# Performance work log

Hardware: AMD Instinct MI355X
Metric: run time of the kernel (lower is better)

The kernel has to match this reference:

```python
import jax, jax.numpy as jnp
import numpy as np

N, E, L, D, ED, M = 100000, 1600000, 4, 64, 16, 128
BN_EPS = 1e-5


def _bn(x, w, b):
    # BatchNorm1d in training mode: biased batch stats over the node dim
    m = x.mean(0)
    v = jnp.mean((x - m) ** 2, axis=0)
    return (x - m) * jax.lax.rsqrt(v + BN_EPS) * w + b


def _leaky(x):
    return jnp.where(x > 0, x, 0.01 * x)  # torch LeakyReLU default slope


def setup_inputs() -> dict:
    key = jax.random.key(0)
    ks = jax.random.split(key, 8)
    s = 0.05
    return {
        "x": jax.random.normal(ks[0], (N, D), jnp.float32),
        "edge_index": jax.random.randint(ks[1], (2, E), 0, N, jnp.int32),
        "edge_attr": jax.random.normal(ks[2], (E, ED), jnp.float32),
        "bn_pre_w": jnp.ones((L, D), jnp.float32),
        "bn_pre_b": jnp.zeros((L, D), jnp.float32),
        "edge_lin_w": jax.random.normal(ks[3], (L, D, ED), jnp.float32) * s,
        "edge_lin_b": jnp.zeros((L, D), jnp.float32),
        "lin1_w": jax.random.normal(ks[4], (L, D, D), jnp.float32) * s,
        "lin1_b": jnp.zeros((L, D), jnp.float32),
        "bn_mid_w": jnp.ones((L, D), jnp.float32),
        "bn_mid_b": jnp.zeros((L, D), jnp.float32),
        "lin2_w": jax.random.normal(ks[5], (L, D, D), jnp.float32) * s,
        "lin2_b": jnp.zeros((L, D), jnp.float32),
        "eps": jnp.zeros((L,), jnp.float32),
        "cls1_w": jax.random.normal(ks[6], (M, D), jnp.float32) * s,
        "cls1_b": jnp.zeros((M,), jnp.float32),
        "cls_bn_w": jnp.ones((M,), jnp.float32),
        "cls_bn_b": jnp.zeros((M,), jnp.float32),
        "cls2_w": jax.random.normal(ks[7], (1, M), jnp.float32) * s,
        "cls2_b": jnp.zeros((1,), jnp.float32),
    }


def reference(x, edge_index, edge_attr, bn_pre_w, bn_pre_b, edge_lin_w, edge_lin_b,
              lin1_w, lin1_b, bn_mid_w, bn_mid_b, lin2_w, lin2_b, eps,
              cls1_w, cls1_b, cls_bn_w, cls_bn_b, cls2_w, cls2_b):
    src, dst = edge_index[0], edge_index[1]
    h = x
    for i in range(L):  # fixed, small layer count
        hn = _bn(h, bn_pre_w[i], bn_pre_b[i])
        hi = hn if i == 0 else _leaky(hn)
        # GINEConv: msg = relu(x_src + Lin(edge_attr)); sum-aggregate at dst
        e = edge_attr @ edge_lin_w[i].T + edge_lin_b[i]            # [E, D]
        msg = jax.nn.relu(hi[src] + e)                              # gather [E, D]
        aggr = jax.ops.segment_sum(msg, dst, num_segments=N)        # scatter [N, D]
        z = (1.0 + eps[i]) * hi + aggr
        # nn: Linear -> BN -> LeakyReLU -> Linear
        z = z @ lin1_w[i].T + lin1_b[i]
        z = _leaky(_bn(z, bn_mid_w[i], bn_mid_b[i]))
        z = z @ lin2_w[i].T + lin2_b[i]
        h = z if i == 0 else h + z  # residual (skipped on first layer)
    y = _leaky(_bn(h @ cls1_w.T + cls1_b, cls_bn_w, cls_bn_b))
    y = y @ cls2_w.T + cls2_b
    return y.reshape(-1)  # torch.flatten -> [N]
```

## Files before the change

kernel.cpp:

```cpp
#include <hip/hip_runtime.h>
#include <hip/hip_bf16.h>

constexpr int GN = 100000;
constexpr int GE = 1600000;
constexpr float FN = 100000.0f;
constexpr float BN_EPS = 1e-5f;

typedef __attribute__((ext_vector_type(8))) short bf16x8;
typedef __attribute__((ext_vector_type(4))) float f32x4;
typedef __bf16 bfp2 __attribute__((ext_vector_type(2)));

#if __has_builtin(__builtin_amdgcn_fdot2_f32_bf16)
#define HAVE_DOT2 1
#else
#define HAVE_DOT2 0
#endif

__device__ __forceinline__ unsigned packbf2(float a, float b) {
    __hip_bfloat162 h = __float22bfloat162_rn(float2{a, b});
    union { __hip_bfloat162 h2; unsigned u; } cv;
    cv.h2 = h;
    return cv.u;
}

__device__ __forceinline__ unsigned short bf16rn(float f) {
    unsigned u = __builtin_bit_cast(unsigned, f);
    unsigned r = (u + 0x7FFF + ((u >> 16) & 1)) >> 16;
    return (unsigned short)r;
}

__device__ __forceinline__ float bflo(unsigned u) {
    return __builtin_bit_cast(float, u << 16);
}
__device__ __forceinline__ float bfhi(unsigned u) {
    return __builtin_bit_cast(float, u & 0xFFFF0000u);
}
__device__ __forceinline__ float bfu16(unsigned short u) {
    return __builtin_bit_cast(float, (unsigned)u << 16);
}


__global__ __launch_bounds__(256) void hist_kernel(const int* __restrict__ dst,
                                                   int* __restrict__ deg) {
    for (int i = blockIdx.x * blockDim.x + threadIdx.x; i < GE; i += gridDim.x * blockDim.x)
        atomicAdd(&deg[dst[i]], 1);
}

__global__ __launch_bounds__(256) void bsum_kernel(const int* __restrict__ deg,
                                                   int* __restrict__ bsum,
                                                   const float* __restrict__ l1w,
                                                   const float* __restrict__ l2w,
                                                   const float* __restrict__ c1w,
                                                   unsigned short* __restrict__ wb) {
    int b = blockIdx.x;
    int i0 = b * 1024 + threadIdx.x * 4;
    int s = 0;
#pragma unroll
    for (int k = 0; k < 4; ++k) {
        int i = i0 + k;
        if (i < GN) s += deg[i];
    }
    for (int o = 32; o >= 1; o >>= 1) s += __shfl_down(s, o, 64);
    __shared__ int ws[4];
    if ((threadIdx.x & 63) == 0) ws[threadIdx.x >> 6] = s;
    __syncthreads();
    if (threadIdx.x == 0) bsum[b] = ws[0] + ws[1] + ws[2] + ws[3];
    for (int i = b * 256 + threadIdx.x; i < 40960; i += gridDim.x * 256) {
        float v;
        if (i < 16384) v = l1w[i];
        else if (i < 32768) v = l2w[i - 16384];
        else v = c1w[i - 32768];
        wb[i] = bf16rn(v);
    }
}

__global__ void bscan_kernel(const int* __restrict__ bsum, int* __restrict__ bbase,
                             int* __restrict__ offEnd, int nb) {
    int t = threadIdx.x;
    int carry = 0;
    for (int base = 0; base < nb; base += 64) {
        int v = (base + t < nb) ? bsum[base + t] : 0;
        int incl = v;
        for (int o = 1; o < 64; o <<= 1) {
            int u = __shfl_up(incl, o, 64);
            if (t >= o) incl += u;
        }
        if (base + t < nb) bbase[base + t] = carry + incl - v;
        carry += __shfl(incl, 63, 64);
    }
    if (t == 0) offEnd[0] = carry;
}

__global__ __launch_bounds__(256) void bscatter_kernel(int* __restrict__ deg,
                                                       const int* __restrict__ bbase,
                                                       int* __restrict__ off) {
    int b = blockIdx.x;
    int t = threadIdx.x;
    int i0 = b * 1024 + t * 4;
    int v[4];
    int s = 0;
#pragma unroll
    for (int k = 0; k < 4; ++k) {
        int i = i0 + k;
        v[k] = (i < GN) ? deg[i] : 0;
        s += v[k];
    }
    int incl = s;
    int lane = t & 63;
    for (int o = 1; o < 64; o <<= 1) {
        int u = __shfl_up(incl, o, 64);
        if (lane >= o) incl += u;
    }
    __shared__ int wsum[4];
    if (lane == 63) wsum[t >> 6] = incl;
    __syncthreads();
    int w = t >> 6;
    int wb = 0;
#pragma unroll
    for (int k = 0; k < 4; ++k)
        if (k < w) wb += wsum[k];
    int ex = bbase[b] + wb + incl - s;
#pragma unroll
    for (int k = 0; k < 4; ++k) {
        int i = i0 + k;
        if (i < GN) { off[i] = ex; deg[i] = ex; }
        ex += v[k];
    }
}

__global__ __launch_bounds__(256) void fill_sorted_kernel(
    const int* __restrict__ src, const int* __restrict__ dst,
    const float4* __restrict__ attr,
    int* __restrict__ cursor,
    int* __restrict__ srcS, unsigned* __restrict__ attrS,
    float* __restrict__ zeroBuf) {
    if (blockIdx.x == 0 && threadIdx.x < 128) zeroBuf[threadIdx.x] = 0.f;
    for (int i = blockIdx.x * blockDim.x + threadIdx.x; i < GE; i += gridDim.x * blockDim.x) {
        int pos = atomicAdd(&cursor[dst[i]], 1);
        srcS[pos] = src[i];
        size_t r = (size_t)i * 4;
        float4 a0 = attr[r], a1 = attr[r + 1], a2 = attr[r + 2], a3 = attr[r + 3];
        uint4 ua, ub;
        ua.x = packbf2(a0.x, a0.y); ua.y = packbf2(a0.z, a0.w);
        ua.z = packbf2(a1.x, a1.y); ua.w = packbf2(a1.z, a1.w);
        ub.x = packbf2(a2.x, a2.y); ub.y = packbf2(a2.z, a2.w);
        ub.z = packbf2(a3.x, a3.y); ub.w = packbf2(a3.z, a3.w);
        uint4* out = (uint4*)(attrS + (size_t)pos * 8);
        out[0] = ua;
        out[1] = ub;
    }
}


__global__ __launch_bounds__(256) void col_stats64(const float* __restrict__ in,
                                                   float* __restrict__ sum,
                                                   float* __restrict__ sq,
                                                   unsigned short* __restrict__ outb) {
    int c = threadIdx.x & 63;
    int lr = threadIdx.x >> 6;
    float s = 0.f, q = 0.f;
    for (int r = blockIdx.x * 4 + lr; r < GN; r += gridDim.x * 4) {
        float v = in[(size_t)r * 64 + c];
        s += v;
        q += v * v;
        outb[(size_t)r * 64 + c] = bf16rn(v);
    }
    __shared__ float S[256];
    S[threadIdx.x] = s;
    __syncthreads();
    if (threadIdx.x < 64) {
        float a = S[threadIdx.x] + S[threadIdx.x + 64] + S[threadIdx.x + 128] + S[threadIdx.x + 192];
        atomicAdd(&sum[threadIdx.x], a);
    }
    __syncthreads();
    S[threadIdx.x] = q;
    __syncthreads();
    if (threadIdx.x < 64) {
        float a = S[threadIdx.x] + S[threadIdx.x + 64] + S[threadIdx.x + 128] + S[threadIdx.x + 192];
        atomicAdd(&sq[threadIdx.x], a);
    }
}


#if HAVE_DOT2
__device__ __forceinline__ float edot(uint4 a, uint4 b, const bfp2* __restrict__ wq,
                                      float e) {
    e = __builtin_amdgcn_fdot2_f32_bf16(__builtin_bit_cast(bfp2, a.x), wq[0], e, false);
    e = __builtin_amdgcn_fdot2_f32_bf16(__builtin_bit_cast(bfp2, a.y), wq[1], e, false);
    e = __builtin_amdgcn_fdot2_f32_bf16(__builtin_bit_cast(bfp2, a.z), wq[2], e, false);
    e = __builtin_amdgcn_fdot2_f32_bf16(__builtin_bit_cast(bfp2, a.w), wq[3], e, false);
    e = __builtin_amdgcn_fdot2_f32_bf16(__builtin_bit_cast(bfp2, b.x), wq[4], e, false);
    e = __builtin_amdgcn_fdot2_f32_bf16(__builtin_bit_cast(bfp2, b.y), wq[5], e, false);
    e = __builtin_amdgcn_fdot2_f32_bf16(__builtin_bit_cast(bfp2, b.z), wq[6], e, false);
    e = __builtin_amdgcn_fdot2_f32_bf16(__builtin_bit_cast(bfp2, b.w), wq[7], e, false);
    return e;
}
#else
__device__ __forceinline__ float edot(uint4 a, uint4 b, const float* __restrict__ w,
                                      float e) {
    e = fmaf(bflo(a.x), w[0], e);  e = fmaf(bfhi(a.x), w[1], e);
    e = fmaf(bflo(a.y), w[2], e);  e = fmaf(bfhi(a.y), w[3], e);
    e = fmaf(bflo(a.z), w[4], e);  e = fmaf(bfhi(a.z), w[5], e);
    e = fmaf(bflo(a.w), w[6], e);  e = fmaf(bfhi(a.w), w[7], e);
    e = fmaf(bflo(b.x), w[8], e);  e = fmaf(bfhi(b.x), w[9], e);
    e = fmaf(bflo(b.y), w[10], e); e = fmaf(bfhi(b.y), w[11], e);
    e = fmaf(bflo(b.z), w[12], e); e = fmaf(bfhi(b.z), w[13], e);
    e = fmaf(bflo(b.w), w[14], e); e = fmaf(bfhi(b.w), w[15], e);
    return e;
}
#endif

__global__ __launch_bounds__(256) void aggregate_kernel(
    const float* __restrict__ h,
    const unsigned short* __restrict__ hb,
    const float* __restrict__ sumv, const float* __restrict__ sqv,
    const float* __restrict__ bnw, const float* __restrict__ bnb,
    int leaky,
    const int* __restrict__ off,
    const int* __restrict__ srcS,
    const unsigned* __restrict__ attrS,
    const float* __restrict__ Wle, const float* __restrict__ ble,
    const float* __restrict__ epsArr, int layer,
    unsigned short* __restrict__ zb,
    float* __restrict__ zeroBuf) {
    if (blockIdx.x == 0 && threadIdx.x < 128) zeroBuf[threadIdx.x] = 0.f;
    const int d = threadIdx.x & 63;
    const int node = __builtin_amdgcn_readfirstlane(blockIdx.x * 4 + (threadIdx.x >> 6));

    float mean = sumv[d] / FN;
    float var = sqv[d] / FN - mean * mean;
    float cA = rsqrtf(var + BN_EPS) * bnw[d];
    float cB = bnb[d] - mean * cA;

#if HAVE_DOT2
    bfp2 wq[8];
#pragma unroll
    for (int k = 0; k < 8; ++k) {
        float2 t = *(const float2*)(Wle + d * 16 + k * 2);
        bfp2 v = {(__bf16)t.x, (__bf16)t.y};
        wq[k] = v;
    }
#else
    float wq[16];
#pragma unroll
    for (int k = 0; k < 16; k += 4) {
        float4 t = *(const float4*)(Wle + d * 16 + k);
        wq[k] = t.x; wq[k + 1] = t.y; wq[k + 2] = t.z; wq[k + 3] = t.w;
    }
#endif
    float be = ble[d];
    float epsv = 1.0f + epsArr[layer];

    int p0 = off[node], p1 = off[node + 1];
    float hv = h[(size_t)node * 64 + d];

    float acc = 0.0f;
    int p = p0;
    int pfull = p0 + ((p1 - p0) & ~7);
    for (; p < pfull; p += 8) {
        int idx[8];
#pragma unroll
        for (int j = 0; j < 8; ++j) idx[j] = srcS[p + j];
        float g[8];
#pragma unroll
        for (int j = 0; j < 8; ++j)
            g[j] = bfu16(hb[(((unsigned)idx[j]) << 6) + d]);
#pragma unroll
        for (int j = 0; j < 8; ++j) {
            const uint4* ar = (const uint4*)(attrS + (size_t)(p + j) * 8);
            float e = edot(ar[0], ar[1], wq, be);
            float gg = g[j] * cA + cB;
            if (leaky) gg = fmaxf(gg, 0.01f * gg);
            acc += fmaxf(gg + e, 0.f);
        }
    }
    for (; p < p1; p += 4) {
        int idx[4];
#pragma unroll
        for (int j = 0; j < 4; ++j) {
            int q = p + j;
            if (q > p1 - 1) q = p1 - 1;
            idx[j] = srcS[q];
        }
        float g[4];
#pragma unroll
        for (int j = 0; j < 4; ++j)
            g[j] = bfu16(hb[(((unsigned)idx[j]) << 6) + d]);
#pragma unroll
        for (int j = 0; j < 4; ++j) {
            int q = p + j;
            if (q > p1 - 1) q = p1 - 1;
            const uint4* ar = (const uint4*)(attrS + (size_t)q * 8);
            float e = edot(ar[0], ar[1], wq, be);
            float gg = g[j] * cA + cB;
            if (leaky) gg = fmaxf(gg, 0.01f * gg);
            float m = fmaxf(gg + e, 0.f);
            acc += (p + j < p1) ? m : 0.f;
        }
    }
    hv = hv * cA + cB;
    if (leaky) hv = fmaxf(hv, 0.01f * hv);
    zb[(size_t)node * 64 + d] = bf16rn(epsv * hv + acc);
}


template <bool BN_IN, bool ABF16, bool STATS, bool RESID, bool BF16OUT, bool F32OUT>
__global__ __launch_bounds__(256) void gemm_mfma(
    const float* __restrict__ srcf, const unsigned short* __restrict__ srcb, int src_ld,
    const unsigned short* __restrict__ Wb,
    const float* __restrict__ bias,
    float* __restrict__ dst, int dst_ld,
    unsigned short* __restrict__ dstb, int dstb_ld,
    const float* __restrict__ resid,
    const float* __restrict__ statsInSum, const float* __restrict__ statsInSq,
    const float* __restrict__ bnw, const float* __restrict__ bnb,
    float* __restrict__ statsOutSum, float* __restrict__ statsOutSq,
    float* __restrict__ zeroBuf, int zeroN) {
    __shared__ float cA[64], cB[64];
    __shared__ float sS[64], sQ[64];
    int tid = threadIdx.x;
    if (zeroBuf && blockIdx.x == 0 && blockIdx.y == 0 && tid < zeroN) zeroBuf[tid] = 0.f;
    int c0 = blockIdx.y * 64;

    if (BN_IN) {
        if (tid < 64) {
            float m = statsInSum[tid] / FN;
            float v = statsInSq[tid] / FN - m * m;
            float a = rsqrtf(v + BN_EPS) * bnw[tid];
            cA[tid] = a;
            cB[tid] = bnb[tid] - m * a;
        }
        __syncthreads();
    }

    int w = tid >> 6, lane = tid & 63;
    int n16 = lane & 15, quad = lane >> 4;

    bf16x8 bfr[4][2];
#pragma unroll
    for (int t = 0; t < 4; ++t) {
        int col = c0 + t * 16 + n16;
        const unsigned short* bsrc = Wb + (size_t)col * 64 + quad * 8;
#pragma unroll
        for (int kk = 0; kk < 2; ++kk)
            bfr[t][kk] = *(const bf16x8*)(bsrc + kk * 32);
    }

    float ls[4] = {0.f, 0.f, 0.f, 0.f}, lq[4] = {0.f, 0.f, 0.f, 0.f};
    constexpr int NT = (GN + 63) / 64;
    for (int tile = blockIdx.x; tile < NT; tile += gridDim.x) {
        int r0 = tile * 64;
        int arow = r0 + w * 16 + n16;
        int arc = arow < GN ? arow : 0;

        bf16x8 afr[2];
        if (ABF16) {
            const unsigned short* asrc = srcb + (size_t)arc * src_ld + quad * 8;
#pragma unroll
            for (int kk = 0; kk < 2; ++kk)
                afr[kk] = *(const bf16x8*)(asrc + kk * 32);
        } else {
            const float* asrc = srcf + (size_t)arc * src_ld + quad * 8;
#pragma unroll
            for (int kk = 0; kk < 2; ++kk) {
                const float4* p = (const float4*)(asrc + kk * 32);
                float4 x0 = p[0], x1 = p[1];
                float av[8] = {x0.x, x0.y, x0.z, x0.w, x1.x, x1.y, x1.z, x1.w};
                if (BN_IN) {
                    int kb = quad * 8 + kk * 32;
#pragma unroll
                    for (int j = 0; j < 8; ++j) {
                        float t = av[j] * cA[kb + j] + cB[kb + j];
                        av[j] = fmaxf(t, 0.01f * t);
                    }
                }
                uint4 fu;
                fu.x = packbf2(av[0], av[1]); fu.y = packbf2(av[2], av[3]);
                fu.z = packbf2(av[4], av[5]); fu.w = packbf2(av[6], av[7]);
                afr[kk] = __builtin_bit_cast(bf16x8, fu);
            }
        }

        f32x4 acc[4] = {{0.f, 0.f, 0.f, 0.f}, {0.f, 0.f, 0.f, 0.f},
                        {0.f, 0.f, 0.f, 0.f}, {0.f, 0.f, 0.f, 0.f}};
#pragma unroll
        for (int t = 0; t < 4; ++t) {
            acc[t] = __builtin_amdgcn_mfma_f32_16x16x32_bf16(afr[0], bfr[t][0], acc[t], 0, 0, 0);
            acc[t] = __builtin_amdgcn_mfma_f32_16x16x32_bf16(afr[1], bfr[t][1], acc[t], 0, 0, 0);
        }

#pragma unroll
        for (int t = 0; t < 4; ++t) {
            int col = c0 + t * 16 + n16;
            float bv = bias[col];
#pragma unroll
            for (int r = 0; r < 4; ++r) {
                int row = r0 + w * 16 + quad * 4 + r;
                if (row < GN) {
                    float o = acc[t][r] + bv;
                    if (RESID) o += resid[(size_t)row * dst_ld + col];
                    if (F32OUT) dst[(size_t)row * dst_ld + col] = o;
                    if (BF16OUT) dstb[(size_t)row * dstb_ld + col] = bf16rn(o);
                    if (STATS) { ls[t] += o; lq[t] += o * o; }
                }
            }
        }
    }

    if (STATS) {
        if (tid < 64) { sS[tid] = 0.f; sQ[tid] = 0.f; }
        __syncthreads();
#pragma unroll
        for (int t = 0; t < 4; ++t) {
            float s = ls[t], q = lq[t];
            s += __shfl_down(s, 16, 64); s += __shfl_down(s, 32, 64);
            q += __shfl_down(q, 16, 64); q += __shfl_down(q, 32, 64);
            if (lane < 16) {
                atomicAdd(&sS[t * 16 + n16], s);
                atomicAdd(&sQ[t * 16 + n16], q);
            }
        }
        __syncthreads();
        if (tid < 64) {
            atomicAdd(&statsOutSum[c0 + tid], sS[tid]);
            atomicAdd(&statsOutSq[c0 + tid], sQ[tid]);
        }
    }
}


__global__ __launch_bounds__(256) void cls2_kernel(
    const unsigned short* __restrict__ y1b,
    const float* __restrict__ sum, const float* __restrict__ sq,
    const float* __restrict__ bnw, const float* __restrict__ bnb,
    const float* __restrict__ w2, const float* __restrict__ b2,
    float* __restrict__ out) {
    int node = blockIdx.x * 4 + (threadIdx.x >> 6);
    int d = threadIdx.x & 63;
    if (node >= GN) return;
    float partial = 0.f;
#pragma unroll
    for (int hh = 0; hh < 2; ++hh) {
        int c = d + hh * 64;
        float m = sum[c] / FN;
        float var = sq[c] / FN - m * m;
        float a = rsqrtf(var + BN_EPS) * bnw[c];
        float v = bfu16(y1b[(size_t)node * 128 + c]);
        v = v * a + (bnb[c] - m * a);
        v = fmaxf(v, 0.01f * v);
        partial += v * w2[c];
    }
    for (int o = 32; o >= 1; o >>= 1) partial += __shfl_down(partial, o, 64);
    if (d == 0) out[node] = partial + b2[0];
}


extern "C" void kernel_launch(void* const* d_in, const int* in_sizes, int n_in,
                              void* d_out, int out_size, void* d_ws, size_t ws_size,
                              hipStream_t stream) {
    (void)in_sizes; (void)n_in; (void)out_size; (void)ws_size;
    const float* x    = (const float*)d_in[0];
    const int*   ei   = (const int*)d_in[1];
    const float* attr = (const float*)d_in[2];
    const float* bnpw = (const float*)d_in[3];
    const float* bnpb = (const float*)d_in[4];
    const float* elw  = (const float*)d_in[5];
    const float* elb  = (const float*)d_in[6];
    const float* l1w  = (const float*)d_in[7];
    const float* l1b  = (const float*)d_in[8];
    const float* bnmw = (const float*)d_in[9];
    const float* bnmb = (const float*)d_in[10];
    const float* l2w  = (const float*)d_in[11];
    const float* l2b  = (const float*)d_in[12];
    const float* epsA = (const float*)d_in[13];
    const float* c1w  = (const float*)d_in[14];
    const float* c1b  = (const float*)d_in[15];
    const float* cbw  = (const float*)d_in[16];
    const float* cbb  = (const float*)d_in[17];
    const float* c2w  = (const float*)d_in[18];
    const float* c2b  = (const float*)d_in[19];
    const int* srcArr = ei;
    const int* dstArr = ei + GE;

    char* base = (char*)d_ws;
    size_t ofs = 0;
    auto alloc = [&](size_t bytes) {
        void* p = base + ofs;
        ofs = (ofs + bytes + 1023) & ~(size_t)1023;
        return p;
    };
    int* off              = (int*)alloc((size_t)(GN + 1) * 4);
    int* cursor           = (int*)alloc((size_t)GN * 4);
    int* src_sorted       = (int*)alloc((size_t)GE * 4);
    unsigned* attr_sorted = (unsigned*)alloc((size_t)GE * 32);
    unsigned short* wbf   = (unsigned short*)alloc(40960 * 2);
    int* bsum   = (int*)alloc(1024);
    int* bbase  = (int*)alloc(1024);
    float* stP0 = (float*)alloc(512);
    float* stP1 = (float*)alloc(512);
    float* stM  = (float*)alloc(512);
    float* stC  = (float*)alloc(1024);
    float* h = (float*)alloc((size_t)GN * 256);
    float* z = (float*)alloc((size_t)GN * 256);
    unsigned short* zb = (unsigned short*)alloc((size_t)GN * 128);
    unsigned short* xb = (unsigned short*)alloc((size_t)GN * 128);
    unsigned short* hb = (unsigned short*)alloc((size_t)GN * 128);
    unsigned short* y1b = (unsigned short*)attr_sorted;

    constexpr int NB = (GN + 1023) / 1024;
    float* stP[2] = {stP0, stP1};

    hipMemsetAsync(cursor, 0, (size_t)GN * 4, stream);
    hist_kernel<<<2048, 256, 0, stream>>>(dstArr, cursor);
    bsum_kernel<<<NB, 256, 0, stream>>>(cursor, bsum, l1w, l2w, c1w, wbf);
    bscan_kernel<<<1, 64, 0, stream>>>(bsum, bbase, off + GN, NB);
    bscatter_kernel<<<NB, 256, 0, stream>>>(cursor, bbase, off);
    fill_sorted_kernel<<<2048, 256, 0, stream>>>(srcArr, dstArr, (const float4*)attr,
                                                 cursor, src_sorted, attr_sorted, stP0);

    col_stats64<<<512, 256, 0, stream>>>(x, stP0, stP0 + 64, xb);

    const float* hsrc = x;
    const unsigned short* hbsrc = xb;
    dim3 gg(782, 1);
    for (int i = 0; i < 4; ++i) {
        float* sIn = stP[i & 1];
        float* sNext = stP[(i + 1) & 1];
        aggregate_kernel<<<25000, 256, 0, stream>>>(
            hsrc, hbsrc, sIn, sIn + 64, bnpw + i * 64, bnpb + i * 64, (i > 0) ? 1 : 0,
            off, src_sorted, attr_sorted, elw + i * 1024, elb + i * 64, epsA, i,
            zb, stM);
        gemm_mfma<false, true, true, false, false, true><<<gg, 256, 0, stream>>>(
            nullptr, zb, 64, wbf + i * 4096, l1b + i * 64, z, 64, nullptr, 0, nullptr,
            nullptr, nullptr, nullptr, nullptr, stM, stM + 64,
            (i == 3) ? stC : sNext, (i == 3) ? 256 : 128);
        if (i == 0)
            gemm_mfma<true, false, true, false, true, true><<<gg, 256, 0, stream>>>(
                z, nullptr, 64, wbf + 16384 + i * 4096, l2b + i * 64, h, 64, hb, 64,
                nullptr, stM, stM + 64, bnmw + i * 64, bnmb + i * 64,
                sNext, sNext + 64, nullptr, 0);
        else if (i < 3)
            gemm_mfma<true, false, true, true, true, true><<<gg, 256, 0, stream>>>(
                z, nullptr, 64, wbf + 16384 + i * 4096, l2b + i * 64, h, 64, hb, 64,
                h, stM, stM + 64, bnmw + i * 64, bnmb + i * 64,
                sNext, sNext + 64, nullptr, 0);
        else
            gemm_mfma<true, false, false, true, true, true><<<gg, 256, 0, stream>>>(
                z, nullptr, 64, wbf + 16384 + i * 4096, l2b + i * 64, h, 64, hb, 64,
                h, stM, stM + 64, bnmw + i * 64, bnmb + i * 64,
                nullptr, nullptr, nullptr, 0);
        hsrc = h;
        hbsrc = hb;
    }

    dim3 gc(391, 2);
    gemm_mfma<false, true, true, false, true, false><<<gc, 256, 0, stream>>>(
        nullptr, hb, 64, wbf + 32768, c1b, nullptr, 128, y1b, 128, nullptr,
        nullptr, nullptr, nullptr, nullptr, stC, stC + 128, nullptr, 0);
    cls2_kernel<<<25000, 256, 0, stream>>>(y1b, stC, stC + 128, cbw, cbb, c2w, c2b,
                                           (float*)d_out);
}
```

Before: 1.004 ms.

## Split edge sort into id scatter plus gather, keep intermediates in bf16

Edge sorting now happens in two passes. The first scatters only edge ids into CSR order. The second gathers src and attr in sorted order and writes them sequentially, replacing scattered 32-byte writes. The GEMM between lin1 and lin2 now writes a bf16 intermediate and reads it back, applying BN and leaky on the bf16 input, instead of a fp32 buffer. The aggregate kernel reads the self term from bf16 hb instead of fp32 h, and the last layer no longer writes fp32 h. This adds an extra pass and buffer for the sort and more bf16 rounding in exchange for less memory traffic.

```diff
diff --git a/kernel.cpp b/kernel.cpp
--- a/kernel.cpp
+++ b/kernel.cpp
@@ -128,24 +128,33 @@
     }
 }
 
-__global__ __launch_bounds__(256) void fill_sorted_kernel(
-    const int* __restrict__ src, const int* __restrict__ dst,
-    const float4* __restrict__ attr,
-    int* __restrict__ cursor,
-    int* __restrict__ srcS, unsigned* __restrict__ attrS,
-    float* __restrict__ zeroBuf) {
+__global__ __launch_bounds__(256) void fill_lite_kernel(const int* __restrict__ dst,
+                                                        int* __restrict__ cursor,
+                                                        int* __restrict__ eids,
+                                                        float* __restrict__ zeroBuf) {
     if (blockIdx.x == 0 && threadIdx.x < 128) zeroBuf[threadIdx.x] = 0.f;
     for (int i = blockIdx.x * blockDim.x + threadIdx.x; i < GE; i += gridDim.x * blockDim.x) {
         int pos = atomicAdd(&cursor[dst[i]], 1);
-        srcS[pos] = src[i];
-        size_t r = (size_t)i * 4;
-        float4 a0 = attr[r], a1 = attr[r + 1], a2 = attr[r + 2], a3 = attr[r + 3];
+        eids[pos] = i;
+    }
+}
+
+__global__ __launch_bounds__(256) void reorder_kernel(const int* __restrict__ eids,
+                                                      const int* __restrict__ src,
+                                                      const float4* __restrict__ attr,
+                                                      int* __restrict__ srcS,
+                                                      unsigned* __restrict__ attrS) {
+    for (int p = blockIdx.x * blockDim.x + threadIdx.x; p < GE; p += gridDim.x * blockDim.x) {
+        int eid = eids[p];
+        srcS[p] = src[eid];
+        const float4* a = attr + (size_t)eid * 4;
+        float4 a0 = a[0], a1 = a[1], a2 = a[2], a3 = a[3];
         uint4 ua, ub;
         ua.x = packbf2(a0.x, a0.y); ua.y = packbf2(a0.z, a0.w);
         ua.z = packbf2(a1.x, a1.y); ua.w = packbf2(a1.z, a1.w);
         ub.x = packbf2(a2.x, a2.y); ub.y = packbf2(a2.z, a2.w);
         ub.z = packbf2(a3.x, a3.y); ub.w = packbf2(a3.z, a3.w);
-        uint4* out = (uint4*)(attrS + (size_t)pos * 8);
+        uint4* out = (uint4*)(attrS + (size_t)p * 8);
         out[0] = ua;
         out[1] = ub;
     }
@@ -211,7 +220,6 @@
 #endif
 
 __global__ __launch_bounds__(256) void aggregate_kernel(
-    const float* __restrict__ h,
     const unsigned short* __restrict__ hb,
     const float* __restrict__ sumv, const float* __restrict__ sqv,
     const float* __restrict__ bnw, const float* __restrict__ bnb,
@@ -252,7 +260,7 @@
     float epsv = 1.0f + epsArr[layer];
 
     int p0 = off[node], p1 = off[node + 1];
-    float hv = h[(size_t)node * 64 + d];
+    float hv = bfu16(hb[(((unsigned)node) << 6) + d]);
 
     float acc = 0.0f;
     int p = p0;
@@ -357,8 +365,24 @@
         if (ABF16) {
             const unsigned short* asrc = srcb + (size_t)arc * src_ld + quad * 8;
 #pragma unroll
-            for (int kk = 0; kk < 2; ++kk)
-                afr[kk] = *(const bf16x8*)(asrc + kk * 32);
+            for (int kk = 0; kk < 2; ++kk) {
+                bf16x8 raw = *(const bf16x8*)(asrc + kk * 32);
+                if (BN_IN) {
+                    int kb = quad * 8 + kk * 32;
+                    float av[8];
+#pragma unroll
+                    for (int j = 0; j < 8; ++j) {
+                        float t = bfu16((unsigned short)raw[j]) * cA[kb + j] + cB[kb + j];
+                        av[j] = fmaxf(t, 0.01f * t);
+                    }
+                    uint4 fu;
+                    fu.x = packbf2(av[0], av[1]); fu.y = packbf2(av[2], av[3]);
+                    fu.z = packbf2(av[4], av[5]); fu.w = packbf2(av[6], av[7]);
+                    afr[kk] = __builtin_bit_cast(bf16x8, fu);
+                } else {
+                    afr[kk] = raw;
+                }
+            }
         } else {
             const float* asrc = srcf + (size_t)arc * src_ld + quad * 8;
 #pragma unroll
@@ -491,6 +515,7 @@
     };
     int* off              = (int*)alloc((size_t)(GN + 1) * 4);
     int* cursor           = (int*)alloc((size_t)GN * 4);
+    int* eids             = (int*)alloc((size_t)GE * 4);
     int* src_sorted       = (int*)alloc((size_t)GE * 4);
     unsigned* attr_sorted = (unsigned*)alloc((size_t)GE * 32);
     unsigned short* wbf   = (unsigned short*)alloc(40960 * 2);
@@ -501,8 +526,8 @@
     float* stM  = (float*)alloc(512);
     float* stC  = (float*)alloc(1024);
     float* h = (float*)alloc((size_t)GN * 256);
-    float* z = (float*)alloc((size_t)GN * 256);
     unsigned short* zb = (unsigned short*)alloc((size_t)GN * 128);
+    unsigned short* tb = (unsigned short*)alloc((size_t)GN * 128);
     unsigned short* xb = (unsigned short*)alloc((size_t)GN * 128);
     unsigned short* hb = (unsigned short*)alloc((size_t)GN * 128);
     unsigned short* y1b = (unsigned short*)attr_sorted;
@@ -515,41 +540,40 @@
     bsum_kernel<<<NB, 256, 0, stream>>>(cursor, bsum, l1w, l2w, c1w, wbf);
     bscan_kernel<<<1, 64, 0, stream>>>(bsum, bbase, off + GN, NB);
     bscatter_kernel<<<NB, 256, 0, stream>>>(cursor, bbase, off);
-    fill_sorted_kernel<<<2048, 256, 0, stream>>>(srcArr, dstArr, (const float4*)attr,
-                                                 cursor, src_sorted, attr_sorted, stP0);
+    fill_lite_kernel<<<2048, 256, 0, stream>>>(dstArr, cursor, eids, stP0);
+    reorder_kernel<<<2048, 256, 0, stream>>>(eids, srcArr, (const float4*)attr,
+                                             src_sorted, attr_sorted);
 
     col_stats64<<<512, 256, 0, stream>>>(x, stP0, stP0 + 64, xb);
 
-    const float* hsrc = x;
     const unsigned short* hbsrc = xb;
     dim3 gg(782, 1);
     for (int i = 0; i < 4; ++i) {
         float* sIn = stP[i & 1];
         float* sNext = stP[(i + 1) & 1];
         aggregate_kernel<<<25000, 256, 0, stream>>>(
-            hsrc, hbsrc, sIn, sIn + 64, bnpw + i * 64, bnpb + i * 64, (i > 0) ? 1 : 0,
+            hbsrc, sIn, sIn + 64, bnpw + i * 64, bnpb + i * 64, (i > 0) ? 1 : 0,
             off, src_sorted, attr_sorted, elw + i * 1024, elb + i * 64, epsA, i,
             zb, stM);
-        gemm_mfma<false, true, true, false, false, true><<<gg, 256, 0, stream>>>(
-            nullptr, zb, 64, wbf + i * 4096, l1b + i * 64, z, 64, nullptr, 0, nullptr,
-            nullptr, nullptr, nullptr, nullptr, stM, stM + 64,
+        gemm_mfma<false, true, true, false, true, false><<<gg, 256, 0, stream>>>(
+            nullptr, zb, 64, wbf + i * 4096, l1b + i * 64, nullptr, 64, tb, 64,
+            nullptr, nullptr, nullptr, nullptr, nullptr, stM, stM + 64,
             (i == 3) ? stC : sNext, (i == 3) ? 256 : 128);
         if (i == 0)
-            gemm_mfma<true, false, true, false, true, true><<<gg, 256, 0, stream>>>(
-                z, nullptr, 64, wbf + 16384 + i * 4096, l2b + i * 64, h, 64, hb, 64,
+            gemm_mfma<true, true, true, false, true, true><<<gg, 256, 0, stream>>>(
+                nullptr, tb, 64, wbf + 16384 + i * 4096, l2b + i * 64, h, 64, hb, 64,
                 nullptr, stM, stM + 64, bnmw + i * 64, bnmb + i * 64,
                 sNext, sNext + 64, nullptr, 0);
         else if (i < 3)
-            gemm_mfma<true, false, true, true, true, true><<<gg, 256, 0, stream>>>(
-                z, nullptr, 64, wbf + 16384 + i * 4096, l2b + i * 64, h, 64, hb, 64,
+            gemm_mfma<true, true, true, true, true, true><<<gg, 256, 0, stream>>>(
+                nullptr, tb, 64, wbf + 16384 + i * 4096, l2b + i * 64, h, 64, hb, 64,
                 h, stM, stM + 64, bnmw + i * 64, bnmb + i * 64,
                 sNext, sNext + 64, nullptr, 0);
         else
-            gemm_mfma<true, false, false, true, true, true><<<gg, 256, 0, stream>>>(
-                z, nullptr, 64, wbf + 16384 + i * 4096, l2b + i * 64, h, 64, hb, 64,
-                h, stM, stM + 64, bnmw + i * 64, bnmb + i * 64,
+            gemm_mfma<true, true, false, true, true, false><<<gg, 256, 0, stream>>>(
+                nullptr, tb, 64, wbf + 16384 + i * 4096, l2b + i * 64, nullptr, 64,
+                hb, 64, h, stM, stM + 64, bnmw + i * 64, bnmb + i * 64,
                 nullptr, nullptr, nullptr, 0);
-        hsrc = h;
         hbsrc = hb;
     }
 
```

Result: slower. 1.063 ms (+5.9%).
